# Performance work log

Measured on AMD Instinct MI355X. Metric: run time of the kernel, lower is better.

Reference implementation:

```python
import math
import jax, jax.numpy as jnp
import numpy as np

H_CYCLES, L_CYCLES = 3, 2
STD = 0.02


def setup_inputs() -> dict:
    key = jax.random.key(0)
    ks = jax.random.split(key, 11)
    D, nh, mult, V, T, B = 512, 8, 64, 8192, 512, 4
    N = mult * D // nh
    def nrm(k, shape):
        return jax.random.normal(k, shape, jnp.float32) * STD
    return {
        "idx": jax.random.randint(ks[0], (B, T), 0, V),
        "embed_w": nrm(ks[1], (V, D)),
        "h_enc": nrm(ks[2], (nh, D, N)),
        "h_enc_v": nrm(ks[3], (nh, D, N)),
        "h_dec": nrm(ks[4], (nh * N, D)),
        "l_enc": nrm(ks[5], (nh, D, N)),
        "l_enc_v": nrm(ks[6], (nh, D, N)),
        "l_dec": nrm(ks[7], (nh * N, D)),
        "lm_head": nrm(ks[8], (D, V)),
        "h_init": nrm(ks[9], (D,)),
        "l_init": nrm(ks[10], (D,)),
    }


def _ln(x, eps=1e-5):
    # LayerNorm without affine params (elementwise_affine=False)
    m = jnp.mean(x, axis=-1, keepdims=True)
    v = jnp.var(x, axis=-1, keepdims=True)
    return (x - m) * jax.lax.rsqrt(v + eps)


def _rope_tables(T, N):
    # freqs with even-quantized exponent, angles wrapped mod 1 then scaled by 2*pi
    q = jnp.floor(jnp.arange(N, dtype=jnp.float32) / 2.0) * 2.0
    freqs = 1.0 / jnp.power(2.0 ** 16, q / N) / (2.0 * math.pi)
    phases = jnp.arange(T, dtype=jnp.float32)[:, None] * freqs[None, :]
    ang = (phases % 1.0) * (2.0 * math.pi)
    return jnp.cos(ang), jnp.sin(ang)  # each (T, N)


def _rope(v, cos, sin):
    # v: (B, nh, T, N); interleaved rotation as in torch stack/view trick
    v_rot = jnp.stack((-v[..., 1::2], v[..., ::2]), axis=-1).reshape(v.shape)
    return v * cos + v_rot * sin


def _attn(x_sparse, Vmat, cos, sin):
    # x_sparse: (B, nh, T, N); Vmat: (B, T, D)
    N = x_sparse.shape[-1]
    T = x_sparse.shape[-2]
    QR = _rope(x_sparse, cos, sin)
    scores = jnp.einsum('bhtn,bhsn->bhts', QR, QR) * (N ** -0.5)
    mask = jnp.tril(jnp.ones((T, T), dtype=bool), k=-1)  # strict lower triangle
    scores = jnp.where(mask, scores, 0.0)
    return jnp.einsum('bhts,bsd->bhtd', scores, Vmat)  # (B, nh, T, D)


def _block(x, inj, enc, enc_v, dec, cos, sin):
    # x, inj: (B, 1, T, D)
    B, _, T, D = x.shape
    nh, _, N = enc.shape
    xi = _ln(x + inj)[:, 0]  # (B, T, D)
    x_sparse = jax.nn.relu(jnp.einsum('btd,hdn->bhtn', xi, enc))
    yKV = _ln(_attn(x_sparse, xi, cos, sin))  # (B, nh, T, D)
    y_sparse = jax.nn.relu(jnp.einsum('bhtd,hdn->bhtn', yKV, enc_v))
    xy = (x_sparse * y_sparse).transpose(0, 2, 1, 3).reshape(B, 1, T, nh * N)
    y = _ln(xy @ dec)  # (B, 1, T, D)
    return _ln(x + y)


def reference(idx, embed_w, h_enc, h_enc_v, h_dec, l_enc, l_enc_v, l_dec,
              lm_head, h_init, l_init):
    B, T = idx.shape
    D = embed_w.shape[1]
    N = l_enc.shape[-1]
    cos, sin = _rope_tables(T, N)
    inp = _ln(embed_w[idx])[:, None]  # (B, 1, T, D)
    z_H = jnp.broadcast_to(h_init, (B, 1, T, D))
    z_L = jnp.broadcast_to(l_init, (B, 1, T, D))
    for h in range(H_CYCLES):
        for l in range(L_CYCLES):
            if not (h == H_CYCLES - 1 and l == L_CYCLES - 1):
                z_L = _block(z_L, z_H + inp, l_enc, l_enc_v, l_dec, cos, sin)
        if h < H_CYCLES - 1:
            z_H = _block(z_H, z_L, h_enc, h_enc_v, h_dec, cos, sin)
    z_L = _block(z_L, z_H + inp, l_enc, l_enc_v, l_dec, cos, sin)
    z_H = _block(z_H, z_L, h_enc, h_enc_v, h_dec, cos, sin)
    logits = z_H[:, 0] @ lm_head  # (B, T, vocab)
    return logits
```

## Files before the change

kernel.cpp:

```cpp
#include <hip/hip_runtime.h>

typedef _Float16 f16;
typedef __attribute__((ext_vector_type(8))) _Float16 f16x8;
typedef __attribute__((ext_vector_type(4))) float f32x4;
typedef __attribute__((ext_vector_type(4))) int i32x4;

#define D_  512
#define NH_ 8
#define NS_ 4096
#define TT_ 512
#define BB_ 4
#define VV_ 8192
#define HN_ 32768
#define BT_ 2048


__device__ __forceinline__ void gl16(const void* g, void* l) {
  __builtin_amdgcn_global_load_lds((const __attribute__((address_space(1))) void*)g,
                                   (__attribute__((address_space(3))) void*)l, 16, 0, 0);
}

__device__ __forceinline__ void gemm_core(const f16* __restrict__ A, const f16* __restrict__ B,
    int lda, int ldb, int nk, char* As, char* Bs, f32x4 acc[4][4]) {
  int tid = threadIdx.x;
  int l = tid & 63, wid = tid >> 6;
  int wm = wid >> 1, wn = wid & 1;
  int row0 = tid >> 3, g0 = tid & 7;
  for (int kt = 0; kt < nk; ++kt) {
    __syncthreads();
#pragma unroll
    for (int it = 0; it < 4; ++it) {
      int row = row0 + 32 * it;
      int gs = g0 ^ (row & 7);
      int wb = (wid * 64 + it * 256) * 16;
      gl16(A + (size_t)row * lda + gs * 8, As + wb);
      gl16(B + (size_t)row * ldb + gs * 8, Bs + wb);
    }
    __syncthreads();
    A += 64; B += 64;
#pragma unroll
    for (int kh = 0; kh < 2; ++kh) {
      f16x8 af[4], bfr[4];
#pragma unroll
      for (int m = 0; m < 4; ++m) {
        int row = wm * 64 + m * 16 + (l & 15);
        af[m] = *(const f16x8*)(As + row * 128 + ((kh * 64 + (l >> 4) * 16) ^ ((row & 7) << 4)));
      }
#pragma unroll
      for (int n = 0; n < 4; ++n) {
        int row = wn * 64 + n * 16 + (l & 15);
        bfr[n] = *(const f16x8*)(Bs + row * 128 + ((kh * 64 + (l >> 4) * 16) ^ ((row & 7) << 4)));
      }
#pragma unroll
      for (int m = 0; m < 4; ++m)
#pragma unroll
        for (int n = 0; n < 4; ++n)
          acc[m][n] = __builtin_amdgcn_mfma_f32_16x16x32_f16(af[m], bfr[n], acc[m][n], 0, 0, 0);
    }
  }
}


__global__ __launch_bounds__(256, 4) void k_gemm_xs(
    const f16* __restrict__ xi, const f16* __restrict__ encT,
    const f16* __restrict__ csT, f16* __restrict__ qr) {
  __shared__ i32x4 As4[1024], Bs4[1024];
  int bid = blockIdx.x;
  int swz = (bid & 7) * 512 + (bid >> 3);
  int mt = swz & 15, nt = (swz >> 4) & 31, h = swz >> 9;
  const f16* A = xi + (size_t)mt * 128 * D_;
  const f16* B = encT + ((size_t)h * NS_ + nt * 128) * D_;
  f32x4 acc[4][4] = {};
  gemm_core(A, B, D_, D_, D_ / 64, (char*)As4, (char*)Bs4, acc);
  int l = threadIdx.x & 63, wid = threadIdx.x >> 6;
  int wm = wid >> 1, wn = wid & 1;
  int r04 = (l >> 4) * 4, c0 = l & 15;
  int b = (mt * 128) >> 9;
  int tbase = (mt * 128) & (TT_ - 1);
#pragma unroll
  for (int m = 0; m < 4; ++m)
#pragma unroll
    for (int n = 0; n < 4; ++n)
#pragma unroll
      for (int r = 0; r < 4; ++r) {
        int row = wm * 64 + m * 16 + r04 + r;
        int col = wn * 64 + n * 16 + c0;
        int t = tbase + row;
        int nn = nt * 128 + col;
        float xsv = fmaxf(acc[m][n][r], 0.f);
        float prt = __shfl_xor(xsv, 1);
        int ci = 2 * (t * NS_ + nn);
        float c = (float)csT[ci], s = (float)csT[ci + 1];
        float qv = xsv * c + ((nn & 1) ? prt : -prt) * s;
        size_t o = (((size_t)b * NH_ + h) * TT_ + t) * NS_ + nn;
        qr[o] = (f16)qv;
      }
}

__global__ __launch_bounds__(256, 4) void k_gemm_scores(
    const f16* __restrict__ qr, f16* __restrict__ scores) {
  __shared__ i32x4 As4[1024], Bs4[1024];
  int bid = blockIdx.x;
  int swz = (bid & 7) * 40 + (bid >> 3);
  int x = swz % 10, z = swz / 10;
  int mt = (x >= 6) ? 3 : (x >= 3) ? 2 : (x >= 1) ? 1 : 0;
  int nt = x - mt * (mt + 1) / 2;
  const f16* base = qr + (size_t)z * TT_ * NS_;
  const f16* A = base + (size_t)mt * 128 * NS_;
  const f16* B = base + (size_t)nt * 128 * NS_;
  f32x4 acc[4][4] = {};
  gemm_core(A, B, NS_, NS_, NS_ / 64, (char*)As4, (char*)Bs4, acc);
  int l = threadIdx.x & 63, wid = threadIdx.x >> 6;
  int wm = wid >> 1, wn = wid & 1;
  int r04 = (l >> 4) * 4, c0 = l & 15;
  f16* outp = scores + (size_t)z * TT_ * TT_;
#pragma unroll
  for (int m = 0; m < 4; ++m)
#pragma unroll
    for (int n = 0; n < 4; ++n)
#pragma unroll
      for (int r = 0; r < 4; ++r) {
        int t = mt * 128 + wm * 64 + m * 16 + r04 + r;
        int s_ = nt * 128 + wn * 64 + n * 16 + c0;
        float v = (t > s_) ? acc[m][n][r] * 0.015625f : 0.f;
        outp[(size_t)t * TT_ + s_] = (f16)v;
      }
}

__global__ __launch_bounds__(256, 4) void k_gemm_attn(
    const f16* __restrict__ scores, const f16* __restrict__ xiT, f16* __restrict__ attn) {
  __shared__ i32x4 As4[1024], Bs4[1024];
  int bid = blockIdx.x;
  int swz = (bid & 7) * 64 + (bid >> 3);
  int mt = swz & 3, ntd = (swz >> 2) & 3, z = swz >> 4;
  int b = z >> 3;
  const f16* A = scores + (size_t)z * TT_ * TT_ + (size_t)mt * 128 * TT_;
  const f16* B = xiT + (size_t)b * D_ * TT_ + (size_t)ntd * 128 * TT_;
  f32x4 acc[4][4] = {};
  gemm_core(A, B, TT_, TT_, 2 * mt + 2, (char*)As4, (char*)Bs4, acc);
  int l = threadIdx.x & 63, wid = threadIdx.x >> 6;
  int wm = wid >> 1, wn = wid & 1;
  int r04 = (l >> 4) * 4, c0 = l & 15;
#pragma unroll
  for (int m = 0; m < 4; ++m)
#pragma unroll
    for (int n = 0; n < 4; ++n)
#pragma unroll
      for (int r = 0; r < 4; ++r) {
        int t = mt * 128 + wm * 64 + m * 16 + r04 + r;
        int d = ntd * 128 + wn * 64 + n * 16 + c0;
        attn[((size_t)z * TT_ + t) * D_ + d] = (f16)acc[m][n][r];
      }
}

__global__ __launch_bounds__(256, 4) void k_gemm_xy(
    const f16* __restrict__ ykv, const f16* __restrict__ encvT,
    const f16* __restrict__ csT, f16* __restrict__ qrxy) {
  __shared__ i32x4 As4[1024], Bs4[1024];
  int bid = blockIdx.x;
  int swz = (bid & 7) * 512 + (bid >> 3);
  int mt = swz & 3, nt = (swz >> 2) & 31, z = swz >> 7;
  int h = z & 7;
  const f16* A = ykv + (size_t)z * TT_ * D_ + (size_t)mt * 128 * D_;
  const f16* B = encvT + ((size_t)h * NS_ + nt * 128) * D_;
  f32x4 acc[4][4] = {};
  gemm_core(A, B, D_, D_, D_ / 64, (char*)As4, (char*)Bs4, acc);
  int l = threadIdx.x & 63, wid = threadIdx.x >> 6;
  int wm = wid >> 1, wn = wid & 1;
  int r04 = (l >> 4) * 4, c0 = l & 15;
#pragma unroll
  for (int m = 0; m < 4; ++m)
#pragma unroll
    for (int n = 0; n < 4; ++n)
#pragma unroll
      for (int r = 0; r < 4; ++r) {
        int t = mt * 128 + wm * 64 + m * 16 + r04 + r;
        int nn = nt * 128 + wn * 64 + n * 16 + c0;
        float ys = fmaxf(acc[m][n][r], 0.f);
        size_t o = ((size_t)z * TT_ + t) * NS_ + nn;
        float qv = (float)qrxy[o];
        float prt = __shfl_xor(qv, 1);
        int ci = 2 * (t * NS_ + nn);
        float c = (float)csT[ci], s = (float)csT[ci + 1];
        float xsv = (nn & 1) ? (qv * c - prt * s) : (qv * c + prt * s);
        qrxy[o] = (f16)(xsv * ys);
      }
}

__global__ __launch_bounds__(256, 4) void k_gemm_ydec(
    const f16* __restrict__ xy, const f16* __restrict__ decT, f16* __restrict__ ypart) {
  __shared__ i32x4 As4[1024], Bs4[1024];
  int bid = blockIdx.x;
  int swz = (bid & 7) * 64 + (bid >> 3);
  int mt = swz & 15, nt = (swz >> 4) & 3, kz = swz >> 6;
  int b = mt >> 2, t0 = (mt & 3) * 128;
  const f16* A = xy + ((size_t)(b * NH_ + kz) * TT_ + t0) * NS_;
  const f16* B = decT + (size_t)nt * 128 * HN_ + (size_t)kz * NS_;
  f32x4 acc[4][4] = {};
  gemm_core(A, B, NS_, HN_, NS_ / 64, (char*)As4, (char*)Bs4, acc);
  int l = threadIdx.x & 63, wid = threadIdx.x >> 6;
  int wm = wid >> 1, wn = wid & 1;
  int r04 = (l >> 4) * 4, c0 = l & 15;
  f16* outp = ypart + (size_t)kz * BT_ * D_;
#pragma unroll
  for (int m = 0; m < 4; ++m)
#pragma unroll
    for (int n = 0; n < 4; ++n)
#pragma unroll
      for (int r = 0; r < 4; ++r) {
        int R = mt * 128 + wm * 64 + m * 16 + r04 + r;
        int c = nt * 128 + wn * 64 + n * 16 + c0;
        outp[(size_t)R * D_ + c] = (f16)acc[m][n][r];
      }
}

__global__ __launch_bounds__(256, 4) void k_gemm_logits(
    const f16* __restrict__ zbf, const f16* __restrict__ lmT, float* __restrict__ outp) {
  __shared__ i32x4 As4[1024], Bs4[1024];
  int bid = blockIdx.x;
  int swz = (bid & 7) * 128 + (bid >> 3);
  int mt = swz & 15, nt = swz >> 4;
  const f16* A = zbf + (size_t)mt * 128 * D_;
  const f16* B = lmT + (size_t)nt * 128 * D_;
  f32x4 acc[4][4] = {};
  gemm_core(A, B, D_, D_, D_ / 64, (char*)As4, (char*)Bs4, acc);
  int l = threadIdx.x & 63, wid = threadIdx.x >> 6;
  int wm = wid >> 1, wn = wid & 1;
  int r04 = (l >> 4) * 4, c0 = l & 15;
#pragma unroll
  for (int m = 0; m < 4; ++m)
#pragma unroll
    for (int n = 0; n < 4; ++n)
#pragma unroll
      for (int r = 0; r < 4; ++r) {
        int R = mt * 128 + wm * 64 + m * 16 + r04 + r;
        int v = nt * 128 + wn * 64 + n * 16 + c0;
        outp[(size_t)R * VV_ + v] = acc[m][n][r];
      }
}


__device__ __forceinline__ float wave_sum(float v) {
#pragma unroll
  for (int o = 32; o > 0; o >>= 1) v += __shfl_xor(v, o);
  return v;
}

__global__ __launch_bounds__(256) void k_tables(f16* __restrict__ csT) {
  int i = blockIdx.x * 256 + threadIdx.x;
  int t = i >> 12, n = i & (NS_ - 1);
  float q = (float)(n & ~1);
  float freq = exp2f(-16.f * q / 4096.f) * 0.15915494309189535f;
  float ph = (float)t * freq;
  ph -= floorf(ph);
  float ang = ph * 6.283185307179586f;
  csT[2 * i]     = (f16)cosf(ang);
  csT[2 * i + 1] = (f16)sinf(ang);
}

__global__ void k_transpose(const float* __restrict__ in, f16* __restrict__ outp, int R, int C) {
  __shared__ float tile[32][33];
  size_t mo = (size_t)blockIdx.z * R * C;
  in += mo; outp += mo;
  int c0 = blockIdx.x * 32, r0 = blockIdx.y * 32;
#pragma unroll
  for (int i = threadIdx.y; i < 32; i += 8)
    tile[i][threadIdx.x] = in[(size_t)(r0 + i) * C + c0 + threadIdx.x];
  __syncthreads();
#pragma unroll
  for (int i = threadIdx.y; i < 32; i += 8)
    outp[(size_t)(c0 + i) * R + r0 + threadIdx.x] = (f16)tile[threadIdx.x][i];
}

__global__ __launch_bounds__(256) void k_embed_ln(const int* __restrict__ idx,
    const float* __restrict__ emb, f16* __restrict__ inp) {
  int r = blockIdx.x * 4 + (threadIdx.x >> 6);
  int lane = threadIdx.x & 63;
  const float* e = emb + (size_t)idx[r] * D_ + lane * 8;
  f32x4 e0 = *(const f32x4*)e;
  f32x4 e1 = *(const f32x4*)(e + 4);
  float v[8];
#pragma unroll
  for (int i = 0; i < 4; ++i) { v[i] = e0[i]; v[i + 4] = e1[i]; }
  float s = 0.f;
#pragma unroll
  for (int i = 0; i < 8; ++i) s += v[i];
  float mean = wave_sum(s) * (1.f / 512.f);
  float q = 0.f;
#pragma unroll
  for (int i = 0; i < 8; ++i) { v[i] -= mean; q += v[i] * v[i]; }
  float rs = rsqrtf(wave_sum(q) * (1.f / 512.f) + 1e-5f);
  f16x8 ov;
#pragma unroll
  for (int i = 0; i < 8; ++i) ov[i] = (f16)(v[i] * rs);
  *(f16x8*)(inp + (size_t)r * D_ + lane * 8) = ov;
}

__global__ __launch_bounds__(256) void k_init(const float* __restrict__ hi,
    const float* __restrict__ li, f16* __restrict__ zH, f16* __restrict__ zL) {
  size_t i = (size_t)blockIdx.x * 256 + threadIdx.x;
  zH[i] = (f16)hi[i & (D_ - 1)];
  zL[i] = (f16)li[i & (D_ - 1)];
}

__global__ __launch_bounds__(256) void k_ln_xi(const f16* __restrict__ x,
    const f16* __restrict__ a1, const f16* __restrict__ a2,
    f16* __restrict__ xi, f16* __restrict__ xiT) {
  int r = blockIdx.x * 4 + (threadIdx.x >> 6);
  int lane = threadIdx.x & 63;
  size_t o = (size_t)r * D_ + lane * 8;
  f16x8 xv = *(const f16x8*)(x + o);
  f16x8 av = *(const f16x8*)(a1 + o);
  float v[8];
#pragma unroll
  for (int i = 0; i < 8; ++i) v[i] = (float)xv[i] + (float)av[i];
  if (a2) {
    f16x8 bv = *(const f16x8*)(a2 + o);
#pragma unroll
    for (int i = 0; i < 8; ++i) v[i] += (float)bv[i];
  }
  float s = 0.f;
#pragma unroll
  for (int i = 0; i < 8; ++i) s += v[i];
  float mean = wave_sum(s) * (1.f / 512.f);
  float q = 0.f;
#pragma unroll
  for (int i = 0; i < 8; ++i) { v[i] -= mean; q += v[i] * v[i]; }
  float rs = rsqrtf(wave_sum(q) * (1.f / 512.f) + 1e-5f);
  f16x8 ov;
#pragma unroll
  for (int i = 0; i < 8; ++i) ov[i] = (f16)(v[i] * rs);
  *(f16x8*)(xi + o) = ov;
  int b = r >> 9, t = r & (TT_ - 1);
  int d0 = lane * 8;
#pragma unroll
  for (int i = 0; i < 8; ++i)
    xiT[((size_t)b * D_ + d0 + i) * TT_ + t] = ov[i];
}

__global__ __launch_bounds__(256) void k_ln_rows(const f16* __restrict__ in, f16* __restrict__ outp) {
  int r = blockIdx.x * 4 + (threadIdx.x >> 6);
  int lane = threadIdx.x & 63;
  size_t o = (size_t)r * D_ + lane * 8;
  f16x8 xv = *(const f16x8*)(in + o);
  float v[8];
#pragma unroll
  for (int i = 0; i < 8; ++i) v[i] = (float)xv[i];
  float s = 0.f;
#pragma unroll
  for (int i = 0; i < 8; ++i) s += v[i];
  float mean = wave_sum(s) * (1.f / 512.f);
  float q = 0.f;
#pragma unroll
  for (int i = 0; i < 8; ++i) { v[i] -= mean; q += v[i] * v[i]; }
  float rs = rsqrtf(wave_sum(q) * (1.f / 512.f) + 1e-5f);
  f16x8 ov;
#pragma unroll
  for (int i = 0; i < 8; ++i) ov[i] = (f16)(v[i] * rs);
  *(f16x8*)(outp + o) = ov;
}

__global__ __launch_bounds__(256) void k_ln_y_out(const f16* __restrict__ ypart,
    f16* __restrict__ z) {
  int r = blockIdx.x * 4 + (threadIdx.x >> 6);
  int lane = threadIdx.x & 63;
  size_t o = (size_t)r * D_ + lane * 8;
  float v[8] = {};
#pragma unroll
  for (int k = 0; k < 8; ++k) {
    f16x8 p = *(const f16x8*)(ypart + (size_t)k * BT_ * D_ + o);
#pragma unroll
    for (int i = 0; i < 8; ++i) v[i] += (float)p[i];
  }
  float s = 0.f;
#pragma unroll
  for (int i = 0; i < 8; ++i) s += v[i];
  float mean = wave_sum(s) * (1.f / 512.f);
  float q = 0.f;
#pragma unroll
  for (int i = 0; i < 8; ++i) { v[i] -= mean; q += v[i] * v[i]; }
  float rs = rsqrtf(wave_sum(q) * (1.f / 512.f) + 1e-5f);
  f16x8 zv = *(const f16x8*)(z + o);
#pragma unroll
  for (int i = 0; i < 8; ++i) v[i] = (float)zv[i] + v[i] * rs;
  s = 0.f;
#pragma unroll
  for (int i = 0; i < 8; ++i) s += v[i];
  mean = wave_sum(s) * (1.f / 512.f);
  q = 0.f;
#pragma unroll
  for (int i = 0; i < 8; ++i) { v[i] -= mean; q += v[i] * v[i]; }
  rs = rsqrtf(wave_sum(q) * (1.f / 512.f) + 1e-5f);
  f16x8 ov;
#pragma unroll
  for (int i = 0; i < 8; ++i) ov[i] = (f16)(v[i] * rs);
  *(f16x8*)(z + o) = ov;
}


extern "C" void kernel_launch(void* const* d_in, const int* in_sizes, int n_in,
                              void* d_out, int out_size, void* d_ws, size_t ws_size,
                              hipStream_t stream) {
  (void)in_sizes; (void)n_in; (void)out_size;
  const int*   idx    = (const int*)  d_in[0];
  const float* emb    = (const float*)d_in[1];
  const float* h_enc  = (const float*)d_in[2];
  const float* h_encv = (const float*)d_in[3];
  const float* h_dec  = (const float*)d_in[4];
  const float* l_enc  = (const float*)d_in[5];
  const float* l_encv = (const float*)d_in[6];
  const float* l_dec  = (const float*)d_in[7];
  const float* lm     = (const float*)d_in[8];
  const float* h_init = (const float*)d_in[9];
  const float* l_init = (const float*)d_in[10];
  float* out = (float*)d_out;

  bool resident = ws_size >= ((size_t)352 << 20);

  char* w = (char*)d_ws;
  size_t off = 0;
  auto alloc = [&](size_t n) { void* p = w + off; off += (n + 255) & ~(size_t)255; return p; };
  f16* csT = (f16*)alloc(8388608);
  f16 *encT[2], *encvT[2], *decT[2], *lmT;
  if (resident) {
    for (int s = 0; s < 2; ++s) {
      encT[s]  = (f16*)alloc(33554432);
      encvT[s] = (f16*)alloc(33554432);
      decT[s]  = (f16*)alloc(33554432);
    }
    lmT = (f16*)alloc(8388608);
  } else {
    encT[0]  = encT[1]  = (f16*)alloc(33554432);
    encvT[0] = encvT[1] = (f16*)alloc(33554432);
    decT[0]  = decT[1]  = (f16*)alloc(33554432);
    lmT = encT[0];
  }
  f16* inp    = (f16*)alloc(2097152);
  f16* zH     = (f16*)alloc(2097152);
  f16* zL     = (f16*)alloc(2097152);
  f16* xi_bf  = (f16*)alloc(2097152);
  f16* xiT_bf = (f16*)alloc(2097152);
  f16* qrxy   = (f16*)alloc(134217728);

  f16* scoresB = (f16*)d_out;
  f16* attnP   = (f16*)((char*)d_out + 16777216);
  f16* ypart   = attnP;
  f16* ykv     = (f16*)((char*)d_out + 33554432);

  dim3 tb(32, 8);
  auto transpose_set = [&](int sel) {
    const float* e  = sel ? h_enc  : l_enc;
    const float* ev = sel ? h_encv : l_encv;
    const float* dc = sel ? h_dec  : l_dec;
    k_transpose<<<dim3(128, 16, 8), tb, 0, stream>>>(e,  encT[sel],  512, 4096);
    k_transpose<<<dim3(128, 16, 8), tb, 0, stream>>>(ev, encvT[sel], 512, 4096);
    k_transpose<<<dim3(16, 1024, 1), tb, 0, stream>>>(dc, decT[sel], 32768, 512);
  };

  k_tables<<<8192, 256, 0, stream>>>(csT);
  k_embed_ln<<<512, 256, 0, stream>>>(idx, emb, inp);
  k_init<<<4096, 256, 0, stream>>>(h_init, l_init, zH, zL);
  if (resident) {
    transpose_set(0);
    transpose_set(1);
    k_transpose<<<dim3(256, 16, 1), tb, 0, stream>>>(lm, lmT, 512, 8192);
  }

  int cur = -1;
  auto setw = [&](int sel) {
    if (resident || cur == sel) { cur = sel; return; }
    cur = sel;
    transpose_set(sel);
  };

  auto run_block = [&](f16* zx, const f16* a1, const f16* a2, int s) {
    k_ln_xi<<<512, 256, 0, stream>>>(zx, a1, a2, xi_bf, xiT_bf);
    k_gemm_xs<<<4096, 256, 0, stream>>>(xi_bf, encT[s], csT, qrxy);
    k_gemm_scores<<<320, 256, 0, stream>>>(qrxy, scoresB);
    k_gemm_attn<<<512, 256, 0, stream>>>(scoresB, xiT_bf, attnP);
    k_ln_rows<<<4096, 256, 0, stream>>>(attnP, ykv);
    k_gemm_xy<<<4096, 256, 0, stream>>>(ykv, encvT[s], csT, qrxy);
    k_gemm_ydec<<<512, 256, 0, stream>>>(qrxy, decT[s], ypart);
    k_ln_y_out<<<512, 256, 0, stream>>>(ypart, zx);
  };

  for (int i = 0; i < 3; ++i) {
    setw(0);
    run_block(zL, inp, zH, 0);
    run_block(zL, inp, zH, 0);
    setw(1);
    run_block(zH, zL, (const f16*)nullptr, 1);
  }
  if (!resident)
    k_transpose<<<dim3(256, 16, 1), tb, 0, stream>>>(lm, lmT, 512, 8192);
  k_gemm_logits<<<1024, 256, 0, stream>>>(zH, lmT, out);
}
```

Before: 4.054 ms.

## Double-buffer GEMM LDS tiles with 32-wide K steps to overlap loads

The shared GEMM core now stages K-slices of 32 into two LDS buffers, prefetching the next slice with global_load_lds while MFMAs run on the current one. This replaces the single-buffer 64-wide K loop, which had two barriers per step and no overlap between global loads and compute. LDS per block stays at 32KB, but there are twice as many iterations, each with a barrier and less MFMA work per barrier. The next-tile load is issued without an explicit wait before the trailing barrier, so correctness relies on the barrier draining outstanding loads.

```diff
diff --git a/kernel.cpp b/kernel.cpp
--- a/kernel.cpp
+++ b/kernel.cpp
@@ -20,43 +20,51 @@
                                    (__attribute__((address_space(3))) void*)l, 16, 0, 0);
 }
 
+__device__ __forceinline__ void stage32(const f16* __restrict__ A, const f16* __restrict__ B,
+                                        int lda, int ldb, char* As, char* Bs) {
+  int tid = threadIdx.x;
+#pragma unroll
+  for (int it = 0; it < 2; ++it) {
+    int ln = tid + 256 * it;
+    int row = ln >> 2, g = ln & 3;
+    int gs = g ^ (row & 3);
+    gl16(A + (size_t)row * lda + gs * 8, As + ln * 16);
+    gl16(B + (size_t)row * ldb + gs * 8, Bs + ln * 16);
+  }
+}
+
 __device__ __forceinline__ void gemm_core(const f16* __restrict__ A, const f16* __restrict__ B,
-    int lda, int ldb, int nk, char* As, char* Bs, f32x4 acc[4][4]) {
+    int lda, int ldb, int nk32, char* sh, f32x4 acc[4][4]) {
   int tid = threadIdx.x;
   int l = tid & 63, wid = tid >> 6;
   int wm = wid >> 1, wn = wid & 1;
-  int row0 = tid >> 3, g0 = tid & 7;
-  for (int kt = 0; kt < nk; ++kt) {
+  stage32(A, B, lda, ldb, sh, sh + 8192);
+  __syncthreads();
+  for (int kt = 0; kt < nk32; ++kt) {
+    int cur = (kt & 1) * 16384;
+    int nxt = cur ^ 16384;
+    if (kt + 1 < nk32)
+      stage32(A + (size_t)(kt + 1) * 32, B + (size_t)(kt + 1) * 32, lda, ldb,
+              sh + nxt, sh + nxt + 8192);
+    const char* As = sh + cur;
+    const char* Bs = sh + cur + 8192;
+    f16x8 af[4], bfr[4];
+#pragma unroll
+    for (int m = 0; m < 4; ++m) {
+      int row = wm * 64 + m * 16 + (l & 15);
+      af[m] = *(const f16x8*)(As + row * 64 + (((l >> 4) * 16) ^ ((row & 3) << 4)));
+    }
+#pragma unroll
+    for (int n = 0; n < 4; ++n) {
+      int row = wn * 64 + n * 16 + (l & 15);
+      bfr[n] = *(const f16x8*)(Bs + row * 64 + (((l >> 4) * 16) ^ ((row & 3) << 4)));
+    }
+#pragma unroll
+    for (int m = 0; m < 4; ++m)
+#pragma unroll
+      for (int n = 0; n < 4; ++n)
+        acc[m][n] = __builtin_amdgcn_mfma_f32_16x16x32_f16(af[m], bfr[n], acc[m][n], 0, 0, 0);
     __syncthreads();
-#pragma unroll
-    for (int it = 0; it < 4; ++it) {
-      int row = row0 + 32 * it;
-      int gs = g0 ^ (row & 7);
-      int wb = (wid * 64 + it * 256) * 16;
-      gl16(A + (size_t)row * lda + gs * 8, As + wb);
-      gl16(B + (size_t)row * ldb + gs * 8, Bs + wb);
-    }
-    __syncthreads();
-    A += 64; B += 64;
-#pragma unroll
-    for (int kh = 0; kh < 2; ++kh) {
-      f16x8 af[4], bfr[4];
-#pragma unroll
-      for (int m = 0; m < 4; ++m) {
-        int row = wm * 64 + m * 16 + (l & 15);
-        af[m] = *(const f16x8*)(As + row * 128 + ((kh * 64 + (l >> 4) * 16) ^ ((row & 7) << 4)));
-      }
-#pragma unroll
-      for (int n = 0; n < 4; ++n) {
-        int row = wn * 64 + n * 16 + (l & 15);
-        bfr[n] = *(const f16x8*)(Bs + row * 128 + ((kh * 64 + (l >> 4) * 16) ^ ((row & 7) << 4)));
-      }
-#pragma unroll
-      for (int m = 0; m < 4; ++m)
-#pragma unroll
-        for (int n = 0; n < 4; ++n)
-          acc[m][n] = __builtin_amdgcn_mfma_f32_16x16x32_f16(af[m], bfr[n], acc[m][n], 0, 0, 0);
-    }
   }
 }
 
@@ -64,14 +72,14 @@
 __global__ __launch_bounds__(256, 4) void k_gemm_xs(
     const f16* __restrict__ xi, const f16* __restrict__ encT,
     const f16* __restrict__ csT, f16* __restrict__ qr) {
-  __shared__ i32x4 As4[1024], Bs4[1024];
+  __shared__ char sh[32768];
   int bid = blockIdx.x;
   int swz = (bid & 7) * 512 + (bid >> 3);
   int mt = swz & 15, nt = (swz >> 4) & 31, h = swz >> 9;
   const f16* A = xi + (size_t)mt * 128 * D_;
   const f16* B = encT + ((size_t)h * NS_ + nt * 128) * D_;
   f32x4 acc[4][4] = {};
-  gemm_core(A, B, D_, D_, D_ / 64, (char*)As4, (char*)Bs4, acc);
+  gemm_core(A, B, D_, D_, D_ / 32, sh, acc);
   int l = threadIdx.x & 63, wid = threadIdx.x >> 6;
   int wm = wid >> 1, wn = wid & 1;
   int r04 = (l >> 4) * 4, c0 = l & 15;
@@ -99,7 +107,7 @@
 
 __global__ __launch_bounds__(256, 4) void k_gemm_scores(
     const f16* __restrict__ qr, f16* __restrict__ scores) {
-  __shared__ i32x4 As4[1024], Bs4[1024];
+  __shared__ char sh[32768];
   int bid = blockIdx.x;
   int swz = (bid & 7) * 40 + (bid >> 3);
   int x = swz % 10, z = swz / 10;
@@ -109,7 +117,7 @@
   const f16* A = base + (size_t)mt * 128 * NS_;
   const f16* B = base + (size_t)nt * 128 * NS_;
   f32x4 acc[4][4] = {};
-  gemm_core(A, B, NS_, NS_, NS_ / 64, (char*)As4, (char*)Bs4, acc);
+  gemm_core(A, B, NS_, NS_, NS_ / 32, sh, acc);
   int l = threadIdx.x & 63, wid = threadIdx.x >> 6;
   int wm = wid >> 1, wn = wid & 1;
   int r04 = (l >> 4) * 4, c0 = l & 15;
@@ -129,7 +137,7 @@
 
 __global__ __launch_bounds__(256, 4) void k_gemm_attn(
     const f16* __restrict__ scores, const f16* __restrict__ xiT, f16* __restrict__ attn) {
-  __shared__ i32x4 As4[1024], Bs4[1024];
+  __shared__ char sh[32768];
   int bid = blockIdx.x;
   int swz = (bid & 7) * 64 + (bid >> 3);
   int mt = swz & 3, ntd = (swz >> 2) & 3, z = swz >> 4;
@@ -137,7 +145,7 @@
   const f16* A = scores + (size_t)z * TT_ * TT_ + (size_t)mt * 128 * TT_;
   const f16* B = xiT + (size_t)b * D_ * TT_ + (size_t)ntd * 128 * TT_;
   f32x4 acc[4][4] = {};
-  gemm_core(A, B, TT_, TT_, 2 * mt + 2, (char*)As4, (char*)Bs4, acc);
+  gemm_core(A, B, TT_, TT_, 4 * mt + 4, sh, acc);
   int l = threadIdx.x & 63, wid = threadIdx.x >> 6;
   int wm = wid >> 1, wn = wid & 1;
   int r04 = (l >> 4) * 4, c0 = l & 15;
@@ -156,7 +164,7 @@
 __global__ __launch_bounds__(256, 4) void k_gemm_xy(
     const f16* __restrict__ ykv, const f16* __restrict__ encvT,
     const f16* __restrict__ csT, f16* __restrict__ qrxy) {
-  __shared__ i32x4 As4[1024], Bs4[1024];
+  __shared__ char sh[32768];
   int bid = blockIdx.x;
   int swz = (bid & 7) * 512 + (bid >> 3);
   int mt = swz & 3, nt = (swz >> 2) & 31, z = swz >> 7;
@@ -164,7 +172,7 @@
   const f16* A = ykv + (size_t)z * TT_ * D_ + (size_t)mt * 128 * D_;
   const f16* B = encvT + ((size_t)h * NS_ + nt * 128) * D_;
   f32x4 acc[4][4] = {};
-  gemm_core(A, B, D_, D_, D_ / 64, (char*)As4, (char*)Bs4, acc);
+  gemm_core(A, B, D_, D_, D_ / 32, sh, acc);
   int l = threadIdx.x & 63, wid = threadIdx.x >> 6;
   int wm = wid >> 1, wn = wid & 1;
   int r04 = (l >> 4) * 4, c0 = l & 15;
@@ -189,7 +197,7 @@
 
 __global__ __launch_bounds__(256, 4) void k_gemm_ydec(
     const f16* __restrict__ xy, const f16* __restrict__ decT, f16* __restrict__ ypart) {
-  __shared__ i32x4 As4[1024], Bs4[1024];
+  __shared__ char sh[32768];
   int bid = blockIdx.x;
   int swz = (bid & 7) * 64 + (bid >> 3);
   int mt = swz & 15, nt = (swz >> 4) & 3, kz = swz >> 6;
@@ -197,7 +205,7 @@
   const f16* A = xy + ((size_t)(b * NH_ + kz) * TT_ + t0) * NS_;
   const f16* B = decT + (size_t)nt * 128 * HN_ + (size_t)kz * NS_;
   f32x4 acc[4][4] = {};
-  gemm_core(A, B, NS_, HN_, NS_ / 64, (char*)As4, (char*)Bs4, acc);
+  gemm_core(A, B, NS_, HN_, NS_ / 32, sh, acc);
   int l = threadIdx.x & 63, wid = threadIdx.x >> 6;
   int wm = wid >> 1, wn = wid & 1;
   int r04 = (l >> 4) * 4, c0 = l & 15;
@@ -216,14 +224,14 @@
 
 __global__ __launch_bounds__(256, 4) void k_gemm_logits(
     const f16* __restrict__ zbf, const f16* __restrict__ lmT, float* __restrict__ outp) {
-  __shared__ i32x4 As4[1024], Bs4[1024];
+  __shared__ char sh[32768];
   int bid = blockIdx.x;
   int swz = (bid & 7) * 128 + (bid >> 3);
   int mt = swz & 15, nt = swz >> 4;
   const f16* A = zbf + (size_t)mt * 128 * D_;
   const f16* B = lmT + (size_t)nt * 128 * D_;
   f32x4 acc[4][4] = {};
-  gemm_core(A, B, D_, D_, D_ / 64, (char*)As4, (char*)Bs4, acc);
+  gemm_core(A, B, D_, D_, D_ / 32, sh, acc);
   int l = threadIdx.x & 63, wid = threadIdx.x >> 6;
   int wm = wid >> 1, wn = wid & 1;
   int r04 = (l >> 4) * 4, c0 = l & 15;
```

After: 4.241 ms. +4.6%, slower.
